# Optimization experiments

Hardware: AMD Instinct MI355X
Metric: run time of the kernel (lower is better)

Reference implementation:

```python
import jax, jax.numpy as jnp
import numpy as np

H = 16          # num_heads
W = 256         # attention_window
D_MODEL = 1024
D_FF = 4096
EPS = 1e-5


def _layernorm(x, g, b):
    mu = jnp.mean(x, axis=-1, keepdims=True)
    var = jnp.mean(jnp.square(x - mu), axis=-1, keepdims=True)
    return (x - mu) * jax.lax.rsqrt(var + EPS) * g + b


def _sliding_attn(q, k, v, w):
    # q,k,v: [B,H,S,d]; each query attends to keys in [i-w, i+w]
    B, Hh, S, d = q.shape
    nc = S // w
    qc = q.reshape(B, Hh, nc, w, d)
    kp = jnp.pad(k, ((0, 0), (0, 0), (w, w), (0, 0)))
    vp = jnp.pad(v, ((0, 0), (0, 0), (w, w), (0, 0)))
    # gather 3w keys per chunk (prev w, current w, next w)
    idx = (jnp.arange(nc) * w)[:, None] + jnp.arange(3 * w)[None, :]  # [nc, 3w]
    kc = kp[:, :, idx, :]  # [B,H,nc,3w,d]
    vc = vp[:, :, idx, :]
    scores = jnp.einsum('bhcqd,bhckd->bhcqk', qc, kc)  # [B,H,nc,w,3w]
    q_pos = jnp.arange(nc)[:, None, None] * w + jnp.arange(w)[None, :, None]
    k_pos = jnp.arange(nc)[:, None, None] * w - w + jnp.arange(3 * w)[None, None, :]
    rel = k_pos - q_pos
    valid = (jnp.abs(rel) <= w) & (k_pos >= 0) & (k_pos < S)  # [nc,w,3w]
    scores = jnp.where(valid[None, None], scores, jnp.float32(-1e9))
    p = jax.nn.softmax(scores, axis=-1)
    out = jnp.einsum('bhcqk,bhckd->bhcqd', p, vc)
    return out.reshape(B, Hh, S, d)


def setup_inputs() -> dict:
    key = jax.random.key(0)
    ks = jax.random.split(key, 8)
    B, S = 2, 4096
    src = jax.random.normal(ks[0], (B, S, D_MODEL), dtype=jnp.float32)
    ln1_g = jnp.ones((D_MODEL,), jnp.float32)
    ln1_b = jnp.zeros((D_MODEL,), jnp.float32)
    ln2_g = jnp.ones((D_MODEL,), jnp.float32)
    ln2_b = jnp.zeros((D_MODEL,), jnp.float32)
    W1 = jax.random.normal(ks[1], (D_MODEL, D_FF), jnp.float32) * 0.02
    b1 = jnp.zeros((D_FF,), jnp.float32)
    W2 = jax.random.normal(ks[2], (D_FF, D_MODEL), jnp.float32) * 0.02
    b2 = jnp.zeros((D_MODEL,), jnp.float32)
    return {"src": src, "ln1_g": ln1_g, "ln1_b": ln1_b, "ln2_g": ln2_g,
            "ln2_b": ln2_b, "W1": W1, "b1": b1, "W2": W2, "b2": b2}


def reference(src, ln1_g, ln1_b, ln2_g, ln2_b, W1, b1, W2, b2):
    B, S, _ = src.shape
    d_head = D_MODEL // H
    qkv = src.reshape(B, S, H, d_head).transpose(0, 2, 1, 3)  # [B,H,S,d]
    attn = _sliding_attn(qkv, qkv, qkv, W)
    attn = attn.transpose(0, 2, 1, 3).reshape(B, S, D_MODEL)
    x = _layernorm(src + attn, ln1_g, ln1_b)
    ff = jnp.maximum(x @ W1 + b1, 0.0) @ W2 + b2
    return _layernorm(x + ff, ln2_g, ln2_b)
```

## Files before the change

### kernel.cpp

```cpp
#include <hip/hip_runtime.h>

typedef __bf16 bf16x8 __attribute__((ext_vector_type(8)));
typedef __bf16 bf16x4 __attribute__((ext_vector_type(4)));
typedef float f32x4 __attribute__((ext_vector_type(4)));

#define MFMA16(a, b, c) __builtin_amdgcn_mfma_f32_16x16x32_bf16((a), (b), (c), 0, 0, 0)

__device__ __forceinline__ void gload_lds16(const void* g, void* l) {
  __builtin_amdgcn_global_load_lds(
      (const __attribute__((address_space(1))) unsigned int*)g,
      (__attribute__((address_space(3))) unsigned int*)l, 16, 0, 0);
}

__global__ __launch_bounds__(512, 2) void attn_kernel(const float* __restrict__ src,
                                                      float* __restrict__ attn_out) {
  const int bid = blockIdx.x;
  const int c = bid & 15;
  const int h = (bid >> 4) & 15;
  const int b = bid >> 8;
  const int tid = threadIdx.x;
  const int w = tid >> 6;
  const int lane = tid & 63;
  const int lg = lane >> 4;
  const int l16 = lane & 15;

  __shared__ __bf16 Ks[64][72];
  __shared__ __bf16 Vt[64][72];

  const int q0 = c * 256 + w * 32;

  bf16x8 qf[2][2];
#pragma unroll
  for (int qfi = 0; qfi < 2; ++qfi)
#pragma unroll
    for (int ks = 0; ks < 2; ++ks) {
      const int row = q0 + qfi * 16 + l16;
      const int d0 = ks * 32 + lg * 8;
      const float* p = src + ((size_t)(b * 4096 + row) * 1024) + h * 64 + d0;
      bf16x8 v;
#pragma unroll
      for (int j = 0; j < 8; ++j) v[j] = (__bf16)p[j];
      qf[qfi][ks] = v;
    }

  int krow[4];
#pragma unroll
  for (int kf = 0; kf < 4; ++kf)
    krow[kf] = ((kf >> 1) << 5) + ((l16 >> 2) << 3) + ((kf & 1) << 2) + (l16 & 3);

  const f32x4 z4 = {0.f, 0.f, 0.f, 0.f};
  float m_run[2], l_run[2];
  f32x4 o[2][4];
#pragma unroll
  for (int qfi = 0; qfi < 2; ++qfi) {
    m_run[qfi] = -6.0e8f;
    l_run[qfi] = 0.f;
#pragma unroll
    for (int df = 0; df < 4; ++df) o[qfi][df] = z4;
  }

  const int stage_key = tid >> 3;
  const int stage_d0 = (tid & 7) * 8;

  for (int kt = 0; kt < 12; ++kt) {
    const int kbase = c * 256 - 256 + kt * 64;
    __syncthreads();
    {
      const int kpos = kbase + stage_key;
      bf16x8 kv;
      if (kpos >= 0 && kpos < 4096) {
        const float* p = src + ((size_t)(b * 4096 + kpos) * 1024) + h * 64 + stage_d0;
#pragma unroll
        for (int j = 0; j < 8; ++j) kv[j] = (__bf16)p[j];
      } else {
#pragma unroll
        for (int j = 0; j < 8; ++j) kv[j] = (__bf16)0.f;
      }
      *(bf16x8*)&Ks[stage_key][stage_d0] = kv;
#pragma unroll
      for (int j = 0; j < 8; ++j) Vt[stage_d0 + j][stage_key] = kv[j];
    }
    __syncthreads();

    const bool skip = (kbase + 63 < 0) | (kbase >= 4096) |
                      (kbase + 63 < q0 - 256) | (kbase > q0 + 31 + 256);
    if (skip) continue;

    f32x4 s[4][2];
#pragma unroll
    for (int kf = 0; kf < 4; ++kf)
#pragma unroll
      for (int qfi = 0; qfi < 2; ++qfi) s[kf][qfi] = z4;

#pragma unroll
    for (int ks = 0; ks < 2; ++ks) {
      bf16x8 ka[4];
#pragma unroll
      for (int kf = 0; kf < 4; ++kf)
        ka[kf] = *(const bf16x8*)&Ks[krow[kf]][ks * 32 + lg * 8];
#pragma unroll
      for (int kf = 0; kf < 4; ++kf)
#pragma unroll
        for (int qfi = 0; qfi < 2; ++qfi)
          s[kf][qfi] = MFMA16(ka[kf], qf[qfi][ks], s[kf][qfi]);
    }

#pragma unroll
    for (int qfi = 0; qfi < 2; ++qfi) {
      const int qp = q0 + qfi * 16 + l16;
#pragma unroll
      for (int kf = 0; kf < 4; ++kf) {
        const int kb0 = kbase + ((kf >> 1) << 5) + 8 * lg + ((kf & 1) << 2);
#pragma unroll
        for (int reg = 0; reg < 4; ++reg) {
          const int kp = kb0 + reg;
          const int rel = kp - qp;
          if (rel > 256 || rel < -256 || kp < 0 || kp >= 4096) s[kf][qfi][reg] = -1e9f;
        }
      }
    }

    bf16x4 pb[4][2];
#pragma unroll
    for (int qfi = 0; qfi < 2; ++qfi) {
      float tm = s[0][qfi][0];
#pragma unroll
      for (int kf = 0; kf < 4; ++kf)
#pragma unroll
        for (int reg = 0; reg < 4; ++reg) tm = fmaxf(tm, s[kf][qfi][reg]);
      tm = fmaxf(tm, __shfl_xor(tm, 16, 64));
      tm = fmaxf(tm, __shfl_xor(tm, 32, 64));

      const float mn = fmaxf(m_run[qfi], tm);
      const float scl = __expf(m_run[qfi] - mn);
      m_run[qfi] = mn;

      float rs = 0.f;
#pragma unroll
      for (int kf = 0; kf < 4; ++kf) {
        bf16x4 pv;
#pragma unroll
        for (int reg = 0; reg < 4; ++reg) {
          const float p = __expf(s[kf][qfi][reg] - mn);
          rs += p;
          pv[reg] = (__bf16)p;
        }
        pb[kf][qfi] = pv;
      }
      rs += __shfl_xor(rs, 16, 64);
      rs += __shfl_xor(rs, 32, 64);
      l_run[qfi] = l_run[qfi] * scl + rs;

#pragma unroll
      for (int df = 0; df < 4; ++df)
#pragma unroll
        for (int reg = 0; reg < 4; ++reg) o[qfi][df][reg] *= scl;
    }

#pragma unroll
    for (int ks2 = 0; ks2 < 2; ++ks2) {
      bf16x8 av[4];
#pragma unroll
      for (int df = 0; df < 4; ++df)
        av[df] = *(const bf16x8*)&Vt[df * 16 + l16][ks2 * 32 + lg * 8];
#pragma unroll
      for (int qfi = 0; qfi < 2; ++qfi) {
        const bf16x8 bq = __builtin_shufflevector(pb[2 * ks2][qfi], pb[2 * ks2 + 1][qfi],
                                                  0, 1, 2, 3, 4, 5, 6, 7);
#pragma unroll
        for (int df = 0; df < 4; ++df)
          o[qfi][df] = MFMA16(av[df], bq, o[qfi][df]);
      }
    }
  }

#pragma unroll
  for (int qfi = 0; qfi < 2; ++qfi) {
    const float inv = 1.0f / l_run[qfi];
    const int qp = q0 + qfi * 16 + l16;
    float* dst = attn_out + ((size_t)(b * 4096 + qp)) * 1024 + h * 64 + lg * 4;
#pragma unroll
    for (int df = 0; df < 4; ++df) {
      float4 r;
      r.x = o[qfi][df][0] * inv;
      r.y = o[qfi][df][1] * inv;
      r.z = o[qfi][df][2] * inv;
      r.w = o[qfi][df][3] * inv;
      *(float4*)&dst[df * 16] = r;
    }
  }
}

template <int MODE>
__global__ __launch_bounds__(512, 2) void gemm8p(const __bf16* __restrict__ A,
                                                 const __bf16* __restrict__ Bt,
                                                 const float* __restrict__ bias,
                                                 void* __restrict__ out,
                                                 int M, int N, int K) {
  __shared__ char smem[147456];
  const int tid = threadIdx.x;
  const int w = tid >> 6;
  const int lane = tid & 63;
  const int lg = lane >> 4;
  const int l16 = lane & 15;
  const int wr = w >> 1;
  const int wc = w & 1;

  const int nbn = N >> 7;
  const int x = ((int)blockIdx.x & 7) * ((int)gridDim.x >> 3) + ((int)blockIdx.x >> 3);
  const long bm = (long)(x / nbn) * 256;
  const long bn = (long)(x % nbn) * 128;

  int ao0 = 0, ao1 = 32768, ao2 = 65536;
  int bo0 = 98304, bo1 = 114688, bo2 = 131072;

  const f32x4 z4 = {0.f, 0.f, 0.f, 0.f};
  f32x4 acc[4][4];
#pragma unroll
  for (int i = 0; i < 4; ++i)
#pragma unroll
    for (int j = 0; j < 4; ++j) acc[i][j] = z4;

  const int srow = tid >> 3;
  const int scsw = ((tid & 7) << 4) ^ ((srow & 7) << 4);
  const char* Ag = (const char*)A + ((size_t)(bm + srow) * K) * 2 + scsw;
  const char* Bg = (const char*)Bt + ((size_t)(bn + srow) * K) * 2 + scsw;
  const size_t ustride = (size_t)K * 128;
  char* lw = smem + (w << 10);

  const unsigned asw = (unsigned)((l16 & 7) << 4);
  const int arow = wr * 64 + l16;
  const int brow = wc * 64 + l16;

  auto stA = [&](int kt, int ao, int u) {
    gload_lds16(Ag + (size_t)u * ustride + (size_t)kt * 128, lw + ao + u * 8192);
  };
  auto stB = [&](int kt, int bo, int v) {
    gload_lds16(Bg + (size_t)v * ustride + (size_t)kt * 128, lw + bo + v * 8192);
  };
  auto rdA = [&](int ao, int rf, int ks) {
    return *(const bf16x8*)(smem + ao + (arow + rf * 16) * 128 +
                            ((unsigned)((ks << 6) | (lg << 4)) ^ asw));
  };
  auto rdB = [&](int bo, int cf, int ks) {
    return *(const bf16x8*)(smem + bo + (brow + cf * 16) * 128 +
                            ((unsigned)((ks << 6) | (lg << 4)) ^ asw));
  };

  const int NT = K >> 6;

#pragma unroll
  for (int u = 0; u < 4; ++u) stA(0, ao0, u);
  stB(0, bo0, 0); stB(0, bo0, 1);
#pragma unroll
  for (int u = 0; u < 4; ++u) stA(1, ao1, u);
  stB(1, bo1, 0); stB(1, bo1, 1);
  asm volatile("s_waitcnt vmcnt(6)" ::: "memory");
  __builtin_amdgcn_s_barrier();

  for (int t = 0; t < NT; ++t) {
    const bool st = (t + 2) < NT;
    const int kt2 = t + 2;
    bf16x8 af[2][2], bl[2][2], bh[2][2];

#pragma unroll
    for (int i = 0; i < 2; ++i)
#pragma unroll
      for (int ks = 0; ks < 2; ++ks) af[i][ks] = rdA(ao0, i, ks);
#pragma unroll
    for (int j = 0; j < 2; ++j)
#pragma unroll
      for (int ks = 0; ks < 2; ++ks) bl[j][ks] = rdB(bo0, j, ks);
    if (st) { stA(kt2, ao2, 0); stA(kt2, ao2, 1); }
    __builtin_amdgcn_s_barrier();
    asm volatile("s_waitcnt lgkmcnt(0)" ::: "memory");
    __builtin_amdgcn_s_setprio(1);
#pragma unroll
    for (int i = 0; i < 2; ++i)
#pragma unroll
      for (int j = 0; j < 2; ++j)
#pragma unroll
        for (int ks = 0; ks < 2; ++ks)
          acc[i][j] = MFMA16(af[i][ks], bl[j][ks], acc[i][j]);
    __builtin_amdgcn_s_setprio(0);
    __builtin_amdgcn_s_barrier();

#pragma unroll
    for (int j = 0; j < 2; ++j)
#pragma unroll
      for (int ks = 0; ks < 2; ++ks) bh[j][ks] = rdB(bo0, 2 + j, ks);
    if (st) { stA(kt2, ao2, 2); stA(kt2, ao2, 3); }
    __builtin_amdgcn_s_barrier();
    asm volatile("s_waitcnt lgkmcnt(0)" ::: "memory");
    __builtin_amdgcn_s_setprio(1);
#pragma unroll
    for (int i = 0; i < 2; ++i)
#pragma unroll
      for (int j = 0; j < 2; ++j)
#pragma unroll
        for (int ks = 0; ks < 2; ++ks)
          acc[i][2 + j] = MFMA16(af[i][ks], bh[j][ks], acc[i][2 + j]);
    __builtin_amdgcn_s_setprio(0);
    __builtin_amdgcn_s_barrier();

#pragma unroll
    for (int i = 0; i < 2; ++i)
#pragma unroll
      for (int ks = 0; ks < 2; ++ks) af[i][ks] = rdA(ao0, 2 + i, ks);
    if (st) stB(kt2, bo2, 0);
    __builtin_amdgcn_s_barrier();
    asm volatile("s_waitcnt lgkmcnt(0)" ::: "memory");
    __builtin_amdgcn_s_setprio(1);
#pragma unroll
    for (int i = 0; i < 2; ++i)
#pragma unroll
      for (int j = 0; j < 2; ++j)
#pragma unroll
        for (int ks = 0; ks < 2; ++ks)
          acc[2 + i][j] = MFMA16(af[i][ks], bl[j][ks], acc[2 + i][j]);
    __builtin_amdgcn_s_setprio(0);
    __builtin_amdgcn_s_barrier();

    if (st) stB(kt2, bo2, 1);
    asm volatile("s_waitcnt vmcnt(6)" ::: "memory");
    __builtin_amdgcn_s_barrier();
    __builtin_amdgcn_s_setprio(1);
#pragma unroll
    for (int i = 0; i < 2; ++i)
#pragma unroll
      for (int j = 0; j < 2; ++j)
#pragma unroll
        for (int ks = 0; ks < 2; ++ks)
          acc[2 + i][2 + j] = MFMA16(af[i][ks], bh[j][ks], acc[2 + i][2 + j]);
    __builtin_amdgcn_s_setprio(0);
    __builtin_amdgcn_s_barrier();

    const int ta = ao0; ao0 = ao1; ao1 = ao2; ao2 = ta;
    const int tb = bo0; bo0 = bo1; bo1 = bo2; bo2 = tb;
  }

  float bv[4];
#pragma unroll
  for (int cf = 0; cf < 4; ++cf) bv[cf] = bias[bn + wc * 64 + cf * 16 + l16];
#pragma unroll
  for (int rf = 0; rf < 4; ++rf)
#pragma unroll
    for (int reg = 0; reg < 4; ++reg) {
      const long row = bm + wr * 64 + rf * 16 + lg * 4 + reg;
#pragma unroll
      for (int cf = 0; cf < 4; ++cf) {
        const long col = bn + wc * 64 + cf * 16 + l16;
        float v = acc[rf][cf][reg] + bv[cf];
        if (MODE == 0) {
          ((__bf16*)out)[row * N + col] = (__bf16)fmaxf(v, 0.f);
        } else {
          ((float*)out)[row * N + col] = v;
        }
      }
    }
}

__global__ __launch_bounds__(256) void transpose_cvt(const float* __restrict__ in,
                                                     __bf16* __restrict__ out,
                                                     int R, int C) {
  __shared__ float tile[64][65];
  const long r0 = (long)blockIdx.y * 64;
  const long c0 = (long)blockIdx.x * 64;
  const int t = threadIdx.x;
  const int tr = t >> 6;
  const int tc = t & 63;
#pragma unroll
  for (int i = 0; i < 16; ++i) {
    const int r = tr * 16 + i;
    tile[r][tc] = in[(r0 + r) * C + c0 + tc];
  }
  __syncthreads();
#pragma unroll
  for (int i = 0; i < 16; ++i) {
    const int cc = tr * 16 + i;
    out[(c0 + cc) * (long)R + r0 + tc] = (__bf16)tile[tc][cc];
  }
}

__global__ __launch_bounds__(256) void ln1_kernel(const float* __restrict__ src,
                                                  const float* __restrict__ attn,
                                                  const float* __restrict__ g,
                                                  const float* __restrict__ bta,
                                                  __bf16* __restrict__ xb) {
  const long r = blockIdx.x;
  const int t = threadIdx.x;
  const float4 a = *(const float4*)&src[r * 1024 + t * 4];
  const float4 cc = *(const float4*)&attn[r * 1024 + t * 4];
  float v[4] = {a.x + cc.x, a.y + cc.y, a.z + cc.z, a.w + cc.w};
  float s = v[0] + v[1] + v[2] + v[3];
  float s2 = v[0] * v[0] + v[1] * v[1] + v[2] * v[2] + v[3] * v[3];
#pragma unroll
  for (int off = 32; off >= 1; off >>= 1) {
    s += __shfl_xor(s, off, 64);
    s2 += __shfl_xor(s2, off, 64);
  }
  __shared__ float red[8];
  if ((t & 63) == 0) { red[t >> 6] = s; red[(t >> 6) + 4] = s2; }
  __syncthreads();
  s = red[0] + red[1] + red[2] + red[3];
  s2 = red[4] + red[5] + red[6] + red[7];
  const float mu = s * (1.f / 1024.f);
  const float var = s2 * (1.f / 1024.f) - mu * mu;
  const float rstd = rsqrtf(var + 1e-5f);
  const float4 gv = *(const float4*)&g[t * 4];
  const float4 bv = *(const float4*)&bta[t * 4];
  bf16x4 y;
  y[0] = (__bf16)((v[0] - mu) * rstd * gv.x + bv.x);
  y[1] = (__bf16)((v[1] - mu) * rstd * gv.y + bv.y);
  y[2] = (__bf16)((v[2] - mu) * rstd * gv.z + bv.z);
  y[3] = (__bf16)((v[3] - mu) * rstd * gv.w + bv.w);
  *(bf16x4*)&xb[r * 1024 + t * 4] = y;
}

__global__ __launch_bounds__(256) void ln2_kernel(const __bf16* __restrict__ xb,
                                                  const float* __restrict__ ff,
                                                  const float* __restrict__ g,
                                                  const float* __restrict__ bta,
                                                  float* __restrict__ out) {
  const long r = blockIdx.x;
  const int t = threadIdx.x;
  const bf16x4 xv = *(const bf16x4*)&xb[r * 1024 + t * 4];
  const float4 fv = *(const float4*)&ff[r * 1024 + t * 4];
  float v[4] = {(float)xv[0] + fv.x, (float)xv[1] + fv.y,
                (float)xv[2] + fv.z, (float)xv[3] + fv.w};
  float s = v[0] + v[1] + v[2] + v[3];
  float s2 = v[0] * v[0] + v[1] * v[1] + v[2] * v[2] + v[3] * v[3];
#pragma unroll
  for (int off = 32; off >= 1; off >>= 1) {
    s += __shfl_xor(s, off, 64);
    s2 += __shfl_xor(s2, off, 64);
  }
  __shared__ float red[8];
  if ((t & 63) == 0) { red[t >> 6] = s; red[(t >> 6) + 4] = s2; }
  __syncthreads();
  s = red[0] + red[1] + red[2] + red[3];
  s2 = red[4] + red[5] + red[6] + red[7];
  const float mu = s * (1.f / 1024.f);
  const float var = s2 * (1.f / 1024.f) - mu * mu;
  const float rstd = rsqrtf(var + 1e-5f);
  const float4 gv = *(const float4*)&g[t * 4];
  const float4 bv = *(const float4*)&bta[t * 4];
  float4 y;
  y.x = (v[0] - mu) * rstd * gv.x + bv.x;
  y.y = (v[1] - mu) * rstd * gv.y + bv.y;
  y.z = (v[2] - mu) * rstd * gv.z + bv.z;
  y.w = (v[3] - mu) * rstd * gv.w + bv.w;
  *(float4*)&out[r * 1024 + t * 4] = y;
}

extern "C" void kernel_launch(void* const* d_in, const int* in_sizes, int n_in,
                              void* d_out, int out_size, void* d_ws, size_t ws_size,
                              hipStream_t stream) {
  const float* src = (const float*)d_in[0];
  const float* ln1_g = (const float*)d_in[1];
  const float* ln1_b = (const float*)d_in[2];
  const float* ln2_g = (const float*)d_in[3];
  const float* ln2_b = (const float*)d_in[4];
  const float* W1 = (const float*)d_in[5];
  const float* b1 = (const float*)d_in[6];
  const float* W2 = (const float*)d_in[7];
  const float* b2 = (const float*)d_in[8];
  float* out = (float*)d_out;
  char* ws = (char*)d_ws;

  float* attn_ff = (float*)ws;
  __bf16* xb = (__bf16*)(ws + 33554432);
  __bf16* w1t = (__bf16*)(ws + 33554432 + 16777216);
  __bf16* w2t = (__bf16*)(ws + 33554432 + 16777216 + 8388608);
  __bf16* hbuf = (__bf16*)(ws + 67108864);

  int Mc = 8192;
  while (Mc > 512 && (67108864ull + (size_t)Mc * 8192ull) > ws_size) Mc >>= 1;

  transpose_cvt<<<dim3(4096 / 64, 1024 / 64), 256, 0, stream>>>(W1, w1t, 1024, 4096);
  transpose_cvt<<<dim3(1024 / 64, 4096 / 64), 256, 0, stream>>>(W2, w2t, 4096, 1024);
  attn_kernel<<<512, 512, 0, stream>>>(src, attn_ff);
  ln1_kernel<<<8192, 256, 0, stream>>>(src, attn_ff, ln1_g, ln1_b, xb);
  for (int m0 = 0; m0 < 8192; m0 += Mc) {
    gemm8p<0><<<(Mc / 256) * (4096 / 128), 512, 0, stream>>>(
        xb + (size_t)m0 * 1024, w1t, b1, hbuf, Mc, 4096, 1024);
    gemm8p<1><<<(Mc / 256) * (1024 / 128), 512, 0, stream>>>(
        hbuf, w2t, b2, attn_ff + (size_t)m0 * 1024, Mc, 1024, 4096);
  }
  ln2_kernel<<<8192, 256, 0, stream>>>(xb, attn_ff, ln2_g, ln2_b, out);
}
```

Measured before the change: 271.7 us.

## Use 256x256 GEMM tiles with double buffering and split-K for second GEMM

Each GEMM block now computes a 256x256 output tile with 8 waves in a 2x4 layout and twice as many accumulators per wave. The LDS pipeline goes from triple to double buffering, staged in k-halves. The second GEMM splits K into two halves along grid.y, writing two partial fp32 outputs. ln2 sums those partials and adds b2, so the FF2 bias is now applied there instead of in the GEMM epilogue. The larger tiles aim to raise arithmetic intensity per LDS byte. Split-K aims to fill the GPU for the narrow N=1024 GEMM, at the cost of extra register pressure and an additional 32MB partial buffer to read back.

```diff
diff --git a/kernel.cpp b/kernel.cpp
--- a/kernel.cpp
+++ b/kernel.cpp
@@ -195,166 +195,151 @@
 __global__ __launch_bounds__(512, 2) void gemm8p(const __bf16* __restrict__ A,
                                                  const __bf16* __restrict__ Bt,
                                                  const float* __restrict__ bias,
-                                                 void* __restrict__ out,
-                                                 int M, int N, int K) {
-  __shared__ char smem[147456];
+                                                 void* __restrict__ out0,
+                                                 void* __restrict__ out1,
+                                                 int M, int N, int Kstride, int Klen) {
+  __shared__ char smem[131072];
   const int tid = threadIdx.x;
   const int w = tid >> 6;
   const int lane = tid & 63;
   const int lg = lane >> 4;
   const int l16 = lane & 15;
-  const int wr = w >> 1;
-  const int wc = w & 1;
-
-  const int nbn = N >> 7;
+  const int wr = w >> 2;
+  const int wc = w & 3;
+
+  const int nbn = N >> 8;
   const int x = ((int)blockIdx.x & 7) * ((int)gridDim.x >> 3) + ((int)blockIdx.x >> 3);
   const long bm = (long)(x / nbn) * 256;
-  const long bn = (long)(x % nbn) * 128;
-
-  int ao0 = 0, ao1 = 32768, ao2 = 65536;
-  int bo0 = 98304, bo1 = 114688, bo2 = 131072;
+  const long bn = (long)(x % nbn) * 256;
+  const long koff = (long)blockIdx.y * Klen;
+  void* out = blockIdx.y ? out1 : out0;
 
   const f32x4 z4 = {0.f, 0.f, 0.f, 0.f};
-  f32x4 acc[4][4];
-#pragma unroll
-  for (int i = 0; i < 4; ++i)
+  f32x4 acc[8][4];
+#pragma unroll
+  for (int i = 0; i < 8; ++i)
 #pragma unroll
     for (int j = 0; j < 4; ++j) acc[i][j] = z4;
 
-  const int srow = tid >> 3;
-  const int scsw = ((tid & 7) << 4) ^ ((srow & 7) << 4);
-  const char* Ag = (const char*)A + ((size_t)(bm + srow) * K) * 2 + scsw;
-  const char* Bg = (const char*)Bt + ((size_t)(bn + srow) * K) * 2 + scsw;
-  const size_t ustride = (size_t)K * 128;
-  char* lw = smem + (w << 10);
-
-  const unsigned asw = (unsigned)((l16 & 7) << 4);
-  const int arow = wr * 64 + l16;
-  const int brow = wc * 64 + l16;
-
-  auto stA = [&](int kt, int ao, int u) {
-    gload_lds16(Ag + (size_t)u * ustride + (size_t)kt * 128, lw + ao + u * 8192);
+  const int srow = tid >> 2;
+  const int g0 = (tid & 3) ^ ((tid >> 3) & 3);
+  const __bf16* Ag = A + (size_t)(bm + srow) * Kstride + koff + g0 * 8;
+  const __bf16* Bg = Bt + (size_t)(bn + srow) * Kstride + koff + g0 * 8;
+
+  auto stage = [&](int kt, int osel, int isB, int khalf) {
+    const __bf16* src = (isB ? Bg : Ag) + (size_t)kt * 64 + khalf * 32;
+    char* dst = smem + (isB ? 65536 : 0) + osel * 32768 + khalf * 16384 + (w << 10);
+    gload_lds16(src, dst);
+    gload_lds16(src + (size_t)128 * Kstride, dst + 8192);
   };
-  auto stB = [&](int kt, int bo, int v) {
-    gload_lds16(Bg + (size_t)v * ustride + (size_t)kt * 128, lw + bo + v * 8192);
+
+  const int lslot = (lg ^ ((l16 >> 1) & 3)) << 4;
+  const char* pA = smem + (wr * 128 + l16) * 64 + lslot;
+  const char* pB = smem + 65536 + (wc * 64 + l16) * 64 + lslot;
+  auto rdA = [&](int sel, int rf, int ks) {
+    return *(const bf16x8*)(pA + sel * 32768 + ks * 16384 + rf * 1024);
   };
-  auto rdA = [&](int ao, int rf, int ks) {
-    return *(const bf16x8*)(smem + ao + (arow + rf * 16) * 128 +
-                            ((unsigned)((ks << 6) | (lg << 4)) ^ asw));
+  auto rdB = [&](int sel, int cf, int ks) {
+    return *(const bf16x8*)(pB + sel * 32768 + ks * 16384 + cf * 1024);
   };
-  auto rdB = [&](int bo, int cf, int ks) {
-    return *(const bf16x8*)(smem + bo + (brow + cf * 16) * 128 +
-                            ((unsigned)((ks << 6) | (lg << 4)) ^ asw));
-  };
-
-  const int NT = K >> 6;
-
-#pragma unroll
-  for (int u = 0; u < 4; ++u) stA(0, ao0, u);
-  stB(0, bo0, 0); stB(0, bo0, 1);
-#pragma unroll
-  for (int u = 0; u < 4; ++u) stA(1, ao1, u);
-  stB(1, bo1, 0); stB(1, bo1, 1);
-  asm volatile("s_waitcnt vmcnt(6)" ::: "memory");
+
+  const int NT = Klen >> 6;
+
+  stage(0, 0, 0, 0);
+  stage(0, 0, 1, 0);
+  stage(0, 0, 0, 1);
+  stage(0, 0, 1, 1);
+  asm volatile("s_waitcnt vmcnt(4)" ::: "memory");
   __builtin_amdgcn_s_barrier();
 
   for (int t = 0; t < NT; ++t) {
-    const bool st = (t + 2) < NT;
-    const int kt2 = t + 2;
-    bf16x8 af[2][2], bl[2][2], bh[2][2];
-
-#pragma unroll
-    for (int i = 0; i < 2; ++i)
-#pragma unroll
-      for (int ks = 0; ks < 2; ++ks) af[i][ks] = rdA(ao0, i, ks);
-#pragma unroll
-    for (int j = 0; j < 2; ++j)
-#pragma unroll
-      for (int ks = 0; ks < 2; ++ks) bl[j][ks] = rdB(bo0, j, ks);
-    if (st) { stA(kt2, ao2, 0); stA(kt2, ao2, 1); }
+    const int sel = t & 1, osel = sel ^ 1;
+    const bool st = (t + 1) < NT;
+    const int kt1 = t + 1;
+    bf16x8 af[8], b0, b1;
+
+#pragma unroll
+    for (int rf = 0; rf < 8; ++rf) af[rf] = rdA(sel, rf, 0);
+    b0 = rdB(sel, 0, 0);
+    b1 = rdB(sel, 1, 0);
+    if (st) stage(kt1, osel, 0, 0);
     __builtin_amdgcn_s_barrier();
     asm volatile("s_waitcnt lgkmcnt(0)" ::: "memory");
     __builtin_amdgcn_s_setprio(1);
 #pragma unroll
-    for (int i = 0; i < 2; ++i)
-#pragma unroll
-      for (int j = 0; j < 2; ++j)
-#pragma unroll
-        for (int ks = 0; ks < 2; ++ks)
-          acc[i][j] = MFMA16(af[i][ks], bl[j][ks], acc[i][j]);
+    for (int rf = 0; rf < 8; ++rf) {
+      acc[rf][0] = MFMA16(af[rf], b0, acc[rf][0]);
+      acc[rf][1] = MFMA16(af[rf], b1, acc[rf][1]);
+    }
     __builtin_amdgcn_s_setprio(0);
     __builtin_amdgcn_s_barrier();
 
-#pragma unroll
-    for (int j = 0; j < 2; ++j)
-#pragma unroll
-      for (int ks = 0; ks < 2; ++ks) bh[j][ks] = rdB(bo0, 2 + j, ks);
-    if (st) { stA(kt2, ao2, 2); stA(kt2, ao2, 3); }
+    b0 = rdB(sel, 2, 0);
+    b1 = rdB(sel, 3, 0);
+    if (st) stage(kt1, osel, 1, 0);
     __builtin_amdgcn_s_barrier();
     asm volatile("s_waitcnt lgkmcnt(0)" ::: "memory");
     __builtin_amdgcn_s_setprio(1);
 #pragma unroll
-    for (int i = 0; i < 2; ++i)
-#pragma unroll
-      for (int j = 0; j < 2; ++j)
-#pragma unroll
-        for (int ks = 0; ks < 2; ++ks)
-          acc[i][2 + j] = MFMA16(af[i][ks], bh[j][ks], acc[i][2 + j]);
+    for (int rf = 0; rf < 8; ++rf) {
+      acc[rf][2] = MFMA16(af[rf], b0, acc[rf][2]);
+      acc[rf][3] = MFMA16(af[rf], b1, acc[rf][3]);
+    }
     __builtin_amdgcn_s_setprio(0);
-    __builtin_amdgcn_s_barrier();
-
-#pragma unroll
-    for (int i = 0; i < 2; ++i)
-#pragma unroll
-      for (int ks = 0; ks < 2; ++ks) af[i][ks] = rdA(ao0, 2 + i, ks);
-    if (st) stB(kt2, bo2, 0);
+    if (st) asm volatile("s_waitcnt vmcnt(4)" ::: "memory");
+    else    asm volatile("s_waitcnt vmcnt(0)" ::: "memory");
+    __builtin_amdgcn_s_barrier();
+
+#pragma unroll
+    for (int rf = 0; rf < 8; ++rf) af[rf] = rdA(sel, rf, 1);
+    b0 = rdB(sel, 0, 1);
+    b1 = rdB(sel, 1, 1);
+    if (st) stage(kt1, osel, 0, 1);
     __builtin_amdgcn_s_barrier();
     asm volatile("s_waitcnt lgkmcnt(0)" ::: "memory");
     __builtin_amdgcn_s_setprio(1);
 #pragma unroll
-    for (int i = 0; i < 2; ++i)
-#pragma unroll
-      for (int j = 0; j < 2; ++j)
-#pragma unroll
-        for (int ks = 0; ks < 2; ++ks)
-          acc[2 + i][j] = MFMA16(af[i][ks], bl[j][ks], acc[2 + i][j]);
+    for (int rf = 0; rf < 8; ++rf) {
+      acc[rf][0] = MFMA16(af[rf], b0, acc[rf][0]);
+      acc[rf][1] = MFMA16(af[rf], b1, acc[rf][1]);
+    }
     __builtin_amdgcn_s_setprio(0);
     __builtin_amdgcn_s_barrier();
 
-    if (st) stB(kt2, bo2, 1);
-    asm volatile("s_waitcnt vmcnt(6)" ::: "memory");
-    __builtin_amdgcn_s_barrier();
+    b0 = rdB(sel, 2, 1);
+    b1 = rdB(sel, 3, 1);
+    if (st) stage(kt1, osel, 1, 1);
+    __builtin_amdgcn_s_barrier();
+    asm volatile("s_waitcnt lgkmcnt(0)" ::: "memory");
     __builtin_amdgcn_s_setprio(1);
 #pragma unroll
-    for (int i = 0; i < 2; ++i)
-#pragma unroll
-      for (int j = 0; j < 2; ++j)
-#pragma unroll
-        for (int ks = 0; ks < 2; ++ks)
-          acc[2 + i][2 + j] = MFMA16(af[i][ks], bh[j][ks], acc[2 + i][2 + j]);
+    for (int rf = 0; rf < 8; ++rf) {
+      acc[rf][2] = MFMA16(af[rf], b0, acc[rf][2]);
+      acc[rf][3] = MFMA16(af[rf], b1, acc[rf][3]);
+    }
     __builtin_amdgcn_s_setprio(0);
-    __builtin_amdgcn_s_barrier();
-
-    const int ta = ao0; ao0 = ao1; ao1 = ao2; ao2 = ta;
-    const int tb = bo0; bo0 = bo1; bo1 = bo2; bo2 = tb;
+    if (st) asm volatile("s_waitcnt vmcnt(4)" ::: "memory");
+    __builtin_amdgcn_s_barrier();
   }
 
   float bv[4];
-#pragma unroll
-  for (int cf = 0; cf < 4; ++cf) bv[cf] = bias[bn + wc * 64 + cf * 16 + l16];
-#pragma unroll
-  for (int rf = 0; rf < 4; ++rf)
+  if (MODE == 0) {
+#pragma unroll
+    for (int cf = 0; cf < 4; ++cf) bv[cf] = bias[bn + wc * 64 + cf * 16 + l16];
+  }
+#pragma unroll
+  for (int rf = 0; rf < 8; ++rf)
 #pragma unroll
     for (int reg = 0; reg < 4; ++reg) {
-      const long row = bm + wr * 64 + rf * 16 + lg * 4 + reg;
+      const long row = bm + wr * 128 + rf * 16 + lg * 4 + reg;
 #pragma unroll
       for (int cf = 0; cf < 4; ++cf) {
         const long col = bn + wc * 64 + cf * 16 + l16;
-        float v = acc[rf][cf][reg] + bv[cf];
         if (MODE == 0) {
-          ((__bf16*)out)[row * N + col] = (__bf16)fmaxf(v, 0.f);
+          const float v = fmaxf(acc[rf][cf][reg] + bv[cf], 0.f);
+          ((__bf16*)out)[row * N + col] = (__bf16)v;
         } else {
-          ((float*)out)[row * N + col] = v;
+          ((float*)out)[row * N + col] = acc[rf][cf][reg];
         }
       }
     }
@@ -418,16 +403,22 @@
 }
 
 __global__ __launch_bounds__(256) void ln2_kernel(const __bf16* __restrict__ xb,
-                                                  const float* __restrict__ ff,
+                                                  const float* __restrict__ f0,
+                                                  const float* __restrict__ f1,
+                                                  const float* __restrict__ b2,
                                                   const float* __restrict__ g,
                                                   const float* __restrict__ bta,
                                                   float* __restrict__ out) {
   const long r = blockIdx.x;
   const int t = threadIdx.x;
   const bf16x4 xv = *(const bf16x4*)&xb[r * 1024 + t * 4];
-  const float4 fv = *(const float4*)&ff[r * 1024 + t * 4];
-  float v[4] = {(float)xv[0] + fv.x, (float)xv[1] + fv.y,
-                (float)xv[2] + fv.z, (float)xv[3] + fv.w};
+  const float4 f0v = *(const float4*)&f0[r * 1024 + t * 4];
+  const float4 f1v = *(const float4*)&f1[r * 1024 + t * 4];
+  const float4 b2v = *(const float4*)&b2[t * 4];
+  float v[4] = {(float)xv[0] + f0v.x + f1v.x + b2v.x,
+                (float)xv[1] + f0v.y + f1v.y + b2v.y,
+                (float)xv[2] + f0v.z + f1v.z + b2v.z,
+                (float)xv[3] + f0v.w + f1v.w + b2v.w};
   float s = v[0] + v[1] + v[2] + v[3];
   float s2 = v[0] * v[0] + v[1] * v[1] + v[2] * v[2] + v[3] * v[3];
 #pragma unroll
@@ -468,24 +459,27 @@
   float* out = (float*)d_out;
   char* ws = (char*)d_ws;
 
-  float* attn_ff = (float*)ws;
-  __bf16* xb = (__bf16*)(ws + 33554432);
-  __bf16* w1t = (__bf16*)(ws + 33554432 + 16777216);
-  __bf16* w2t = (__bf16*)(ws + 33554432 + 16777216 + 8388608);
-  __bf16* hbuf = (__bf16*)(ws + 67108864);
+  const size_t MB = 1048576;
+  float* ff0 = (float*)ws;
+  float* ff1 = (float*)(ws + 32 * MB);
+  __bf16* xb = (__bf16*)(ws + 64 * MB);
+  __bf16* w1t = (__bf16*)(ws + 80 * MB);
+  __bf16* w2t = (__bf16*)(ws + 88 * MB);
+  __bf16* hbuf = (__bf16*)(ws + 96 * MB);
 
   int Mc = 8192;
-  while (Mc > 512 && (67108864ull + (size_t)Mc * 8192ull) > ws_size) Mc >>= 1;
+  while (Mc > 512 && 96 * MB + (size_t)Mc * 8192 > ws_size) Mc >>= 1;
 
   transpose_cvt<<<dim3(4096 / 64, 1024 / 64), 256, 0, stream>>>(W1, w1t, 1024, 4096);
   transpose_cvt<<<dim3(1024 / 64, 4096 / 64), 256, 0, stream>>>(W2, w2t, 4096, 1024);
-  attn_kernel<<<512, 512, 0, stream>>>(src, attn_ff);
-  ln1_kernel<<<8192, 256, 0, stream>>>(src, attn_ff, ln1_g, ln1_b, xb);
+  attn_kernel<<<512, 512, 0, stream>>>(src, ff0);
+  ln1_kernel<<<8192, 256, 0, stream>>>(src, ff0, ln1_g, ln1_b, xb);
   for (int m0 = 0; m0 < 8192; m0 += Mc) {
-    gemm8p<0><<<(Mc / 256) * (4096 / 128), 512, 0, stream>>>(
-        xb + (size_t)m0 * 1024, w1t, b1, hbuf, Mc, 4096, 1024);
-    gemm8p<1><<<(Mc / 256) * (1024 / 128), 512, 0, stream>>>(
-        hbuf, w2t, b2, attn_ff + (size_t)m0 * 1024, Mc, 1024, 4096);
-  }
-  ln2_kernel<<<8192, 256, 0, stream>>>(xb, attn_ff, ln2_g, ln2_b, out);
-}
+    gemm8p<0><<<dim3((Mc / 256) * (4096 / 256), 1), 512, 0, stream>>>(
+        xb + (size_t)m0 * 1024, w1t, b1, hbuf, hbuf, Mc, 4096, 1024, 1024);
+    gemm8p<1><<<dim3((Mc / 256) * (1024 / 256), 2), 512, 0, stream>>>(
+        hbuf, w2t, nullptr, ff0 + (size_t)m0 * 1024, ff1 + (size_t)m0 * 1024,
+        Mc, 1024, 4096, 2048);
+  }
+  ln2_kernel<<<8192, 256, 0, stream>>>(xb, ff0, ff1, b2, ln2_g, ln2_b, out);
+}
```

After: 256.2 us. 1.06x faster.
